# Kernel tuning notes

Hardware: AMD Instinct MI355X
Metric: run time of the kernel (lower is better)

The kernel has to match this reference:

```python
import jax, jax.numpy as jnp
import numpy as np

NUM_HEADS = 16


def setup_inputs() -> dict:
    key = jax.random.key(0)
    k1, k2, k3 = jax.random.split(key, 3)
    B, L, H = 2, 2048, 1024
    return {
        "key": jax.random.normal(k1, (B, L, H), dtype=jnp.float32),
        "W_ctx": jax.random.normal(k2, (H, H), dtype=jnp.float32) * (1.0 / np.sqrt(H)),
        "b_ctx": jax.random.normal(k3, (H,), dtype=jnp.float32) * 0.01,
    }


def reference(key, W_ctx, b_ctx):
    # Note: the torch module defines q/k/v Linear layers but never calls them
    # in forward(); it reshapes the raw input into heads directly.
    B, L, H = key.shape
    dh = H // NUM_HEADS
    # [B, L, H] -> [B, nh, L, dh]
    x = key.reshape(B, L, NUM_HEADS, dh).transpose(0, 2, 1, 3)
    # QK^T then scale by sqrt(head_dim) (key.shape[-1] after head split)
    scores = jnp.einsum("bhqd,bhkd->bhqk", x, x) * (1.0 / np.float32(np.sqrt(dh)))
    attn = jax.nn.softmax(scores, axis=-1)  # dropout p treated as eval/identity
    ctx = jnp.einsum("bhqk,bhkd->bhqd", attn, x)
    # [B, nh, L, dh] -> [B, L, H]
    ctx = ctx.transpose(0, 2, 1, 3).reshape(B, L, H)
    # context_transform: nn.Linear(H, H, bias=True)
    return ctx @ W_ctx.T + b_ctx
```

## Files before the change

### kernel.cpp

```cpp
#include <hip/hip_runtime.h>
#include <stdint.h>

#define NH     16
#define LSEQ   2048
#define DH     64
#define HDIM   1024
#define BATCH  2

typedef __attribute__((ext_vector_type(8))) short bf16x8;
typedef __attribute__((ext_vector_type(4))) short bf16x4;
typedef __attribute__((ext_vector_type(8))) unsigned short u16x8;
typedef __attribute__((ext_vector_type(4))) float f32x4;
typedef __attribute__((ext_vector_type(16))) float f32x16;

static __device__ inline unsigned short f2bs(float f) {
    union { float f; uint32_t u; } v; v.f = f;
    uint32_t u = v.u;
    return (unsigned short)((u + 0x7FFFu + ((u >> 16) & 1u)) >> 16);
}

static __device__ inline unsigned int cvtpk(float lo, float hi) {
    unsigned int r;
    asm("v_cvt_pk_bf16_f32 %0, %1, %2" : "=v"(r) : "v"(lo), "v"(hi));
    return r;
}
static __device__ inline void pl32swap(unsigned int &a, unsigned int &b) {
    asm volatile("v_permlane32_swap_b32 %0, %1" : "+v"(a), "+v"(b));
}

#define GLOAD_LDS(gp, lp) \
    __builtin_amdgcn_global_load_lds((const __attribute__((address_space(1))) void*)(gp), \
                                     (__attribute__((address_space(3))) void*)(lp), 16, 0, 0)

#define MFMA32(A, B, C) __builtin_amdgcn_mfma_f32_32x32x16_bf16((A), (B), (C), 0, 0, 0)

#define QK_SCALE 0.42466083f

__global__ __launch_bounds__(256) void prep_kernel(const float* __restrict__ x,
                                                   const float* __restrict__ W,
                                                   unsigned short* __restrict__ xb,
                                                   unsigned short* __restrict__ xt,
                                                   unsigned short* __restrict__ wbt) {
    const int lt = blockIdx.x, bh = blockIdx.y;
    const int bid = bh * 32 + lt;
    const int t = threadIdx.x;

    if (t < 128) {
        const int gid = bid * 128 + t;
        const int n  = gid >> 7;
        const int kc = gid & 127;
        const float* src = W + (size_t)n * 1024 + kc * 8;
        float4 f0 = *(const float4*)(src);
        float4 f1 = *(const float4*)(src + 4);
        u16x8 v;
        v[0]=f2bs(f0.x); v[1]=f2bs(f0.y); v[2]=f2bs(f0.z); v[3]=f2bs(f0.w);
        v[4]=f2bs(f1.x); v[5]=f2bs(f1.y); v[6]=f2bs(f1.z); v[7]=f2bs(f1.w);
        const int nt = n >> 7, rn = n & 127;
        const int kt = kc >> 3, c = kc & 7;
        *(u16x8*)(wbt + (((size_t)nt * 16 + kt) * 128 + rn) * 64 + ((c ^ (rn & 7)) * 8)) = v;
    }

    const int b = bh >> 4, h = bh & 15;
    const int r = t >> 2, cp = t & 3;

    __shared__ __align__(16) unsigned short Sm[64][72];

    const float* src = x + ((size_t)(b * LSEQ + lt * 64 + r)) * HDIM + h * DH + cp * 16;
    float4 f0 = *(const float4*)(src);
    float4 f1 = *(const float4*)(src + 4);
    float4 f2 = *(const float4*)(src + 8);
    float4 f3 = *(const float4*)(src + 12);
    u16x8 lo, hi;
    lo[0]=f2bs(f0.x); lo[1]=f2bs(f0.y); lo[2]=f2bs(f0.z); lo[3]=f2bs(f0.w);
    lo[4]=f2bs(f1.x); lo[5]=f2bs(f1.y); lo[6]=f2bs(f1.z); lo[7]=f2bs(f1.w);
    hi[0]=f2bs(f2.x); hi[1]=f2bs(f2.y); hi[2]=f2bs(f2.z); hi[3]=f2bs(f2.w);
    hi[4]=f2bs(f3.x); hi[5]=f2bs(f3.y); hi[6]=f2bs(f3.z); hi[7]=f2bs(f3.w);
    u16x8 slo, shi;
    slo[0]=f2bs(f0.x*QK_SCALE); slo[1]=f2bs(f0.y*QK_SCALE); slo[2]=f2bs(f0.z*QK_SCALE); slo[3]=f2bs(f0.w*QK_SCALE);
    slo[4]=f2bs(f1.x*QK_SCALE); slo[5]=f2bs(f1.y*QK_SCALE); slo[6]=f2bs(f1.z*QK_SCALE); slo[7]=f2bs(f1.w*QK_SCALE);
    shi[0]=f2bs(f2.x*QK_SCALE); shi[1]=f2bs(f2.y*QK_SCALE); shi[2]=f2bs(f2.z*QK_SCALE); shi[3]=f2bs(f2.w*QK_SCALE);
    shi[4]=f2bs(f3.x*QK_SCALE); shi[5]=f2bs(f3.y*QK_SCALE); shi[6]=f2bs(f3.z*QK_SCALE); shi[7]=f2bs(f3.w*QK_SCALE);

    {
        unsigned short* xrow = xb + (size_t)bid * 4096 + r * 64;
        const int xrs = (r & 7) * 8;
        *(u16x8*)(xrow + ((cp * 16 + 0) ^ xrs)) = slo;
        *(u16x8*)(xrow + ((cp * 16 + 8) ^ xrs)) = shi;
    }
    *(u16x8*)&Sm[r][cp * 16]     = lo;
    *(u16x8*)&Sm[r][cp * 16 + 8] = hi;
    __syncthreads();

    {
        const int d = t >> 2, part = (t & 3) * 16;
        unsigned short* vrow = xt + (size_t)bid * 4096 + d * 64;
        const int xrs = (d & 7) * 8;
        u16x8 g0, g1;
        #pragma unroll
        for (int i = 0; i < 8; ++i) g0[i] = Sm[part + i][d];
        #pragma unroll
        for (int i = 0; i < 8; ++i) g1[i] = Sm[part + 8 + i][d];
        *(u16x8*)(vrow + ((part + 0) ^ xrs)) = g0;
        *(u16x8*)(vrow + ((part + 8) ^ xrs)) = g1;
    }
}

__global__ __launch_bounds__(256) void attn_kernel(const unsigned short* __restrict__ xb,
                                                   const unsigned short* __restrict__ xt,
                                                   unsigned short* __restrict__ ctxt) {
    const int bh = blockIdx.x;
    const int qt = blockIdx.y;
    const int tid = threadIdx.x;
    const int w = tid >> 6, lane = tid & 63;
    const int l31 = lane & 31, hh = lane >> 5;

    __shared__ __align__(16) unsigned short KL[4][4096];
    __shared__ __align__(16) unsigned short VL[4][4096];

    const char* xbB = (const char*)(xb + (size_t)bh * 32 * 4096);
    const char* xtB = (const char*)(xt + (size_t)bh * 32 * 4096);

    bf16x8 qf[4];
    {
        const int qtile = qt * 2 + (w >> 1);
        const int rq = (w & 1) * 32 + l31;
        const char* qbase = xbB + (size_t)qtile * 8192 + rq * 128;
        const int qxr = (rq & 7) << 4;
        #pragma unroll
        for (int ds = 0; ds < 4; ++ds)
            qf[ds] = *(const bf16x8*)(qbase + ((ds * 32 + hh * 16) ^ qxr));
    }

    f32x16 accA, accB;
    #pragma unroll
    for (int r = 0; r < 16; ++r) { accA[r] = 0.f; accB[r] = 0.f; }
    float lp = 0.f;

    const int soff = tid * 16;
    #pragma unroll
    for (int j = 0; j < 2; ++j) {
        const char* kps = xbB + j * 8192;
        const char* vps = xtB + j * 8192;
        GLOAD_LDS(kps + soff,        (char*)KL[j] + soff);
        GLOAD_LDS(kps + 4096 + soff, (char*)KL[j] + 4096 + soff);
        GLOAD_LDS(vps + soff,        (char*)VL[j] + soff);
        GLOAD_LDS(vps + 4096 + soff, (char*)VL[j] + 4096 + soff);
    }
    asm volatile("s_waitcnt vmcnt(4)" ::: "memory");
    __builtin_amdgcn_s_barrier();

    const int kxr = (l31 & 7) << 4;

    for (int tt = 0; tt < 32; ++tt) {
        if (tt < 30) {
            const char* kps = xbB + (tt + 2) * 8192;
            const char* vps = xtB + (tt + 2) * 8192;
            char* kdst = (char*)KL[(tt + 2) & 3];
            char* vdst = (char*)VL[(tt + 2) & 3];
            GLOAD_LDS(kps + soff,        kdst + soff);
            GLOAD_LDS(kps + 4096 + soff, kdst + 4096 + soff);
            GLOAD_LDS(vps + soff,        vdst + soff);
            GLOAD_LDS(vps + 4096 + soff, vdst + 4096 + soff);
        }

        const char* kb0 = (const char*)KL[tt & 3] + l31 * 128;
        const char* kb1 = kb0 + 4096;
        f32x16 s0, s1;
        #pragma unroll
        for (int r = 0; r < 16; ++r) { s0[r] = 0.f; s1[r] = 0.f; }
        __builtin_amdgcn_s_setprio(1);
        #pragma unroll
        for (int ds = 0; ds < 4; ++ds) {
            const int off = (ds * 32 + hh * 16) ^ kxr;
            bf16x8 kfa = *(const bf16x8*)(kb0 + off);
            bf16x8 kfb = *(const bf16x8*)(kb1 + off);
            s0 = MFMA32(kfa, qf[ds], s0);
            s1 = MFMA32(kfb, qf[ds], s1);
        }
        __builtin_amdgcn_s_setprio(0);

        f32x16 e0, e1;
        {
            float ls = 0.f;
            #pragma unroll
            for (int r = 0; r < 16; ++r) {
                e0[r] = __builtin_amdgcn_exp2f(s0[r]);
                e1[r] = __builtin_amdgcn_exp2f(s1[r]);
                ls += e0[r] + e1[r];
            }
            lp += ls;
        }
        bf16x8 pa[4];
        #pragma unroll
        for (int ks = 0; ks < 4; ++ks) {
            const int r0 = (ks & 1) * 8;
            unsigned int x0, y0, x1, y1;
            if (ks < 2) {
                x0 = cvtpk(e0[r0 + 0], e0[r0 + 1]);
                y0 = cvtpk(e0[r0 + 4], e0[r0 + 5]);
                x1 = cvtpk(e0[r0 + 2], e0[r0 + 3]);
                y1 = cvtpk(e0[r0 + 6], e0[r0 + 7]);
            } else {
                x0 = cvtpk(e1[r0 + 0], e1[r0 + 1]);
                y0 = cvtpk(e1[r0 + 4], e1[r0 + 5]);
                x1 = cvtpk(e1[r0 + 2], e1[r0 + 3]);
                y1 = cvtpk(e1[r0 + 6], e1[r0 + 7]);
            }
            pl32swap(x0, y0);
            pl32swap(x1, y1);
            union { unsigned int u[4]; bf16x8 v; } pu;
            pu.u[0] = x0; pu.u[1] = x1; pu.u[2] = y0; pu.u[3] = y1;
            pa[ks] = pu.v;
        }

        if (tt < 30) {
            asm volatile("s_waitcnt vmcnt(4)" ::: "memory");
        } else {
            asm volatile("s_waitcnt vmcnt(0)" ::: "memory");
        }
        __builtin_amdgcn_s_barrier();

        const char* vb0 = (const char*)VL[tt & 3] + l31 * 128;
        const char* vb1 = vb0 + 4096;
        __builtin_amdgcn_s_setprio(1);
        #pragma unroll
        for (int ks = 0; ks < 4; ++ks) {
            const int off = (ks * 32 + hh * 16) ^ kxr;
            bf16x8 vfa = *(const bf16x8*)(vb0 + off);
            bf16x8 vfb = *(const bf16x8*)(vb1 + off);
            accA = MFMA32(pa[ks], vfa, accA);
            accB = MFMA32(pa[ks], vfb, accB);
        }
        __builtin_amdgcn_s_setprio(0);
    }

    lp += __shfl_xor(lp, 32);
    const float inv = 1.0f / lp;
    __syncthreads();
    float* invL = (float*)KL;
    invL[w * 32 + l31] = inv;
    __syncthreads();

    const int b = bh >> 4, hd = bh & 15;
    const int mt = b * 16 + qt;
    unsigned short* tbase = ctxt + ((size_t)mt * 16 + hd) * 128 * 64;
    const int col0 = l31, col1 = 32 + l31;
    const int c80 = col0 >> 3, c81 = col1 >> 3, ce = col0 & 7;
    #pragma unroll
    for (int r = 0; r < 16; ++r) {
        const int crow = (r & 3) + 8 * (r >> 2) + 4 * hh;
        const float iv = invL[w * 32 + crow];
        const int rr = w * 32 + crow;
        unsigned short* rowp = tbase + rr * 64;
        const int sw = rr & 7;
        rowp[((c80 ^ sw) * 8) + ce] = f2bs(accA[r] * iv);
        rowp[((c81 ^ sw) * 8) + ce] = f2bs(accB[r] * iv);
    }
}

__global__ __launch_bounds__(256) void proj_kernel(const unsigned short* __restrict__ ctxt,
                                                   const unsigned short* __restrict__ wbt,
                                                   const float* __restrict__ bias,
                                                   float* __restrict__ out) {
    const int ntb = blockIdx.x;
    const int mtb = blockIdx.y;
    const int tid = threadIdx.x;
    const int w = tid >> 6, lane = tid & 63;
    const int la = lane & 15, quad = lane >> 4;
    const int wm = (w >> 1) * 64, wn = (w & 1) * 64;

    __shared__ __align__(16) unsigned short As[2][8192];
    __shared__ __align__(16) unsigned short Bs[2][8192];

    const unsigned short* abase = ctxt + (size_t)mtb * 16 * 8192;
    const unsigned short* bbase = wbt  + (size_t)ntb * 16 * 8192;

    const int sw0 = ((quad)     ^ (la & 7)) * 8;
    const int sw1 = ((quad + 4) ^ (la & 7)) * 8;

    const f32x4 fzero = {0.f, 0.f, 0.f, 0.f};
    f32x4 acc[4][4];
    #pragma unroll
    for (int i = 0; i < 4; ++i)
        #pragma unroll
        for (int j = 0; j < 4; ++j) acc[i][j] = fzero;

    #pragma unroll
    for (int j = 0; j < 4; ++j) {
        const int fc = j * 256 + tid;
        GLOAD_LDS((const char*)abase + fc * 16, (char*)As[0] + fc * 16);
        GLOAD_LDS((const char*)bbase + fc * 16, (char*)Bs[0] + fc * 16);
    }
    __syncthreads();

    for (int kt = 0; kt < 16; ++kt) {
        if (kt < 15) {
            const char* asrc = (const char*)(abase + (kt + 1) * 8192);
            const char* bsrc = (const char*)(bbase + (kt + 1) * 8192);
            char* adst = (char*)As[(kt + 1) & 1];
            char* bdst = (char*)Bs[(kt + 1) & 1];
            #pragma unroll
            for (int j = 0; j < 4; ++j) {
                const int fc = j * 256 + tid;
                GLOAD_LDS(asrc + fc * 16, adst + fc * 16);
                GLOAD_LDS(bsrc + fc * 16, bdst + fc * 16);
            }
        }

        const unsigned short* Ab = As[kt & 1];
        const unsigned short* Bb = Bs[kt & 1];
        #pragma unroll
        for (int ks2 = 0; ks2 < 2; ++ks2) {
            const int sw = ks2 ? sw1 : sw0;
            bf16x8 af[4], bfr[4];
            #pragma unroll
            for (int mt = 0; mt < 4; ++mt) af[mt]  = *(const bf16x8*)&Ab[(wm + mt * 16 + la) * 64 + sw];
            #pragma unroll
            for (int nt = 0; nt < 4; ++nt) bfr[nt] = *(const bf16x8*)&Bb[(wn + nt * 16 + la) * 64 + sw];
            #pragma unroll
            for (int mt = 0; mt < 4; ++mt)
                #pragma unroll
                for (int nt = 0; nt < 4; ++nt)
                    acc[mt][nt] = __builtin_amdgcn_mfma_f32_16x16x32_bf16(af[mt], bfr[nt], acc[mt][nt], 0, 0, 0);
        }
        __syncthreads();
    }

    const int m0 = mtb * 128, n0 = ntb * 128;
    #pragma unroll
    for (int nt = 0; nt < 4; ++nt) {
        const int n = n0 + wn + nt * 16 + la;
        const float bv = bias[n];
        #pragma unroll
        for (int mt = 0; mt < 4; ++mt)
            #pragma unroll
            for (int r = 0; r < 4; ++r) {
                const int m = m0 + wm + mt * 16 + quad * 4 + r;
                out[(size_t)m * HDIM + n] = acc[mt][nt][r] + bv;
            }
    }
}

extern "C" void kernel_launch(void* const* d_in, const int* in_sizes, int n_in,
                              void* d_out, int out_size, void* d_ws, size_t ws_size,
                              hipStream_t stream) {
    const float* x    = (const float*)d_in[0];
    const float* W    = (const float*)d_in[1];
    const float* bias = (const float*)d_in[2];
    float* out = (float*)d_out;

    unsigned short* ctxt = (unsigned short*)d_ws;
    unsigned short* xbp  = (unsigned short*)((char*)d_ws + ( 8u << 20));
    unsigned short* xtp  = (unsigned short*)((char*)d_ws + (16u << 20));
    unsigned short* wbt  = (unsigned short*)((char*)d_ws + (24u << 20));

    prep_kernel<<<dim3(32, 32), 256, 0, stream>>>(x, W, xbp, xtp, wbt);
    attn_kernel<<<dim3(32, 16), 256, 0, stream>>>(xbp, xtp, ctxt);
    proj_kernel<<<dim3(8, 32), 256, 0, stream>>>(ctxt, wbt, bias, out);
}
```

Measured before the change: 144.3 us.

## Load K/V fragments directly from global in MFMA-ready layout, drop LDS staging

The prep kernel now writes K and V^T in a fragment-major layout so each lane can load its MFMA operands straight from global memory with contiguous 16-byte reads. The attention kernel drops the LDS ring buffer, the async global-to-LDS copies and the per-tile barriers. The softmax row sum is now computed with an extra MFMA against a ones vector instead of scalar adds and a shuffle. Occupancy is hinted at 3 blocks per SM. This relies on L2/cache for K/V reuse across the four waves and loses explicit prefetch overlap, and it adds one MFMA per step for the row sum.

Result: no change. 142.8 us (-1.0%).

```diff
diff --git a/kernel.cpp b/kernel.cpp
--- a/kernel.cpp
+++ b/kernel.cpp
@@ -8,7 +8,6 @@
 #define BATCH  2
 
 typedef __attribute__((ext_vector_type(8))) short bf16x8;
-typedef __attribute__((ext_vector_type(4))) short bf16x4;
 typedef __attribute__((ext_vector_type(8))) unsigned short u16x8;
 typedef __attribute__((ext_vector_type(4))) float f32x4;
 typedef __attribute__((ext_vector_type(16))) float f32x16;
@@ -82,10 +81,10 @@
     shi[4]=f2bs(f3.x*QK_SCALE); shi[5]=f2bs(f3.y*QK_SCALE); shi[6]=f2bs(f3.z*QK_SCALE); shi[7]=f2bs(f3.w*QK_SCALE);
 
     {
-        unsigned short* xrow = xb + (size_t)bid * 4096 + r * 64;
-        const int xrs = (r & 7) * 8;
-        *(u16x8*)(xrow + ((cp * 16 + 0) ^ xrs)) = slo;
-        *(u16x8*)(xrow + ((cp * 16 + 8) ^ xrs)) = shi;
+        unsigned short* xbase = xb + (size_t)bh * 131072
+                              + ((size_t)lt * 2 + (r >> 5)) * 2048 + cp * 512 + (r & 31) * 8;
+        *(u16x8*)(xbase)       = slo;
+        *(u16x8*)(xbase + 256) = shi;
     }
     *(u16x8*)&Sm[r][cp * 16]     = lo;
     *(u16x8*)&Sm[r][cp * 16 + 8] = hi;
@@ -93,118 +92,98 @@
 
     {
         const int d = t >> 2, part = (t & 3) * 16;
-        unsigned short* vrow = xt + (size_t)bid * 4096 + d * 64;
-        const int xrs = (d & 7) * 8;
+        unsigned short* vbase = xt + (size_t)bh * 131072 + (size_t)lt * 4096
+                              + (d >> 5) * 2048 + (part >> 4) * 512 + (d & 31) * 8;
         u16x8 g0, g1;
         #pragma unroll
         for (int i = 0; i < 8; ++i) g0[i] = Sm[part + i][d];
         #pragma unroll
         for (int i = 0; i < 8; ++i) g1[i] = Sm[part + 8 + i][d];
-        *(u16x8*)(vrow + ((part + 0) ^ xrs)) = g0;
-        *(u16x8*)(vrow + ((part + 8) ^ xrs)) = g1;
-    }
-}
-
-__global__ __launch_bounds__(256) void attn_kernel(const unsigned short* __restrict__ xb,
-                                                   const unsigned short* __restrict__ xt,
-                                                   unsigned short* __restrict__ ctxt) {
+        *(u16x8*)(vbase)       = g0;
+        *(u16x8*)(vbase + 256) = g1;
+    }
+}
+
+__global__ __launch_bounds__(256, 3) void attn_kernel(const unsigned short* __restrict__ xb,
+                                                      const unsigned short* __restrict__ xt,
+                                                      unsigned short* __restrict__ ctxt) {
     const int bh = blockIdx.x;
     const int qt = blockIdx.y;
     const int tid = threadIdx.x;
     const int w = tid >> 6, lane = tid & 63;
     const int l31 = lane & 31, hh = lane >> 5;
 
-    __shared__ __align__(16) unsigned short KL[4][4096];
-    __shared__ __align__(16) unsigned short VL[4][4096];
-
-    const char* xbB = (const char*)(xb + (size_t)bh * 32 * 4096);
-    const char* xtB = (const char*)(xt + (size_t)bh * 32 * 4096);
+    const char* xbB = (const char*)(xb + (size_t)bh * 131072);
+    const char* xtB = (const char*)(xt + (size_t)bh * 131072);
 
     bf16x8 qf[4];
     {
-        const int qtile = qt * 2 + (w >> 1);
-        const int rq = (w & 1) * 32 + l31;
-        const char* qbase = xbB + (size_t)qtile * 8192 + rq * 128;
-        const int qxr = (rq & 7) << 4;
+        const char* qbase = xbB + (size_t)(qt * 4 + w) * 4096 + lane * 16;
         #pragma unroll
         for (int ds = 0; ds < 4; ++ds)
-            qf[ds] = *(const bf16x8*)(qbase + ((ds * 32 + hh * 16) ^ qxr));
-    }
-
-    f32x16 accA, accB;
-    #pragma unroll
-    for (int r = 0; r < 16; ++r) { accA[r] = 0.f; accB[r] = 0.f; }
-    float lp = 0.f;
-
-    const int soff = tid * 16;
-    #pragma unroll
-    for (int j = 0; j < 2; ++j) {
-        const char* kps = xbB + j * 8192;
-        const char* vps = xtB + j * 8192;
-        GLOAD_LDS(kps + soff,        (char*)KL[j] + soff);
-        GLOAD_LDS(kps + 4096 + soff, (char*)KL[j] + 4096 + soff);
-        GLOAD_LDS(vps + soff,        (char*)VL[j] + soff);
-        GLOAD_LDS(vps + 4096 + soff, (char*)VL[j] + 4096 + soff);
-    }
-    asm volatile("s_waitcnt vmcnt(4)" ::: "memory");
-    __builtin_amdgcn_s_barrier();
-
-    const int kxr = (l31 & 7) << 4;
+            qf[ds] = *(const bf16x8*)(qbase + ds * 1024);
+    }
+
+    bf16x8 ones;
+    #pragma unroll
+    for (int i = 0; i < 8; ++i) ones[i] = (short)0x3F80;
+
+    f32x16 accA, accB, accS;
+    #pragma unroll
+    for (int r = 0; r < 16; ++r) { accA[r] = 0.f; accB[r] = 0.f; accS[r] = 0.f; }
+
+    const char* ka = xbB + lane * 16;
+    const char* va = xtB + lane * 16;
 
     for (int tt = 0; tt < 32; ++tt) {
-        if (tt < 30) {
-            const char* kps = xbB + (tt + 2) * 8192;
-            const char* vps = xtB + (tt + 2) * 8192;
-            char* kdst = (char*)KL[(tt + 2) & 3];
-            char* vdst = (char*)VL[(tt + 2) & 3];
-            GLOAD_LDS(kps + soff,        kdst + soff);
-            GLOAD_LDS(kps + 4096 + soff, kdst + 4096 + soff);
-            GLOAD_LDS(vps + soff,        vdst + soff);
-            GLOAD_LDS(vps + 4096 + soff, vdst + 4096 + soff);
-        }
-
-        const char* kb0 = (const char*)KL[tt & 3] + l31 * 128;
-        const char* kb1 = kb0 + 4096;
+        bf16x8 kfa[4], kfb[4];
+        #pragma unroll
+        for (int ds = 0; ds < 4; ++ds) {
+            kfa[ds] = *(const bf16x8*)(ka + ds * 1024);
+            kfb[ds] = *(const bf16x8*)(ka + 4096 + ds * 1024);
+        }
+
         f32x16 s0, s1;
         #pragma unroll
         for (int r = 0; r < 16; ++r) { s0[r] = 0.f; s1[r] = 0.f; }
         __builtin_amdgcn_s_setprio(1);
         #pragma unroll
         for (int ds = 0; ds < 4; ++ds) {
-            const int off = (ds * 32 + hh * 16) ^ kxr;
-            bf16x8 kfa = *(const bf16x8*)(kb0 + off);
-            bf16x8 kfb = *(const bf16x8*)(kb1 + off);
-            s0 = MFMA32(kfa, qf[ds], s0);
-            s1 = MFMA32(kfb, qf[ds], s1);
+            s0 = MFMA32(kfa[ds], qf[ds], s0);
+            s1 = MFMA32(kfb[ds], qf[ds], s1);
         }
         __builtin_amdgcn_s_setprio(0);
 
-        f32x16 e0, e1;
-        {
-            float ls = 0.f;
-            #pragma unroll
-            for (int r = 0; r < 16; ++r) {
-                e0[r] = __builtin_amdgcn_exp2f(s0[r]);
-                e1[r] = __builtin_amdgcn_exp2f(s1[r]);
-                ls += e0[r] + e1[r];
-            }
-            lp += ls;
-        }
+        bf16x8 vfa[4], vfb[4];
+        #pragma unroll
+        for (int ks = 0; ks < 4; ++ks) {
+            vfa[ks] = *(const bf16x8*)(va + ks * 1024);
+            vfb[ks] = *(const bf16x8*)(va + 4096 + ks * 1024);
+        }
+        ka += 8192;
+        va += 8192;
+
+        #pragma unroll
+        for (int r = 0; r < 16; ++r) {
+            s0[r] = __builtin_amdgcn_exp2f(s0[r]);
+            s1[r] = __builtin_amdgcn_exp2f(s1[r]);
+        }
+
         bf16x8 pa[4];
         #pragma unroll
         for (int ks = 0; ks < 4; ++ks) {
             const int r0 = (ks & 1) * 8;
             unsigned int x0, y0, x1, y1;
             if (ks < 2) {
-                x0 = cvtpk(e0[r0 + 0], e0[r0 + 1]);
-                y0 = cvtpk(e0[r0 + 4], e0[r0 + 5]);
-                x1 = cvtpk(e0[r0 + 2], e0[r0 + 3]);
-                y1 = cvtpk(e0[r0 + 6], e0[r0 + 7]);
+                x0 = cvtpk(s0[r0 + 0], s0[r0 + 1]);
+                y0 = cvtpk(s0[r0 + 4], s0[r0 + 5]);
+                x1 = cvtpk(s0[r0 + 2], s0[r0 + 3]);
+                y1 = cvtpk(s0[r0 + 6], s0[r0 + 7]);
             } else {
-                x0 = cvtpk(e1[r0 + 0], e1[r0 + 1]);
-                y0 = cvtpk(e1[r0 + 4], e1[r0 + 5]);
-                x1 = cvtpk(e1[r0 + 2], e1[r0 + 3]);
-                y1 = cvtpk(e1[r0 + 6], e1[r0 + 7]);
+                x0 = cvtpk(s1[r0 + 0], s1[r0 + 1]);
+                y0 = cvtpk(s1[r0 + 4], s1[r0 + 5]);
+                x1 = cvtpk(s1[r0 + 2], s1[r0 + 3]);
+                y1 = cvtpk(s1[r0 + 6], s1[r0 + 7]);
             }
             pl32swap(x0, y0);
             pl32swap(x1, y1);
@@ -213,43 +192,24 @@
             pa[ks] = pu.v;
         }
 
-        if (tt < 30) {
-            asm volatile("s_waitcnt vmcnt(4)" ::: "memory");
-        } else {
-            asm volatile("s_waitcnt vmcnt(0)" ::: "memory");
-        }
-        __builtin_amdgcn_s_barrier();
-
-        const char* vb0 = (const char*)VL[tt & 3] + l31 * 128;
-        const char* vb1 = vb0 + 4096;
         __builtin_amdgcn_s_setprio(1);
         #pragma unroll
         for (int ks = 0; ks < 4; ++ks) {
-            const int off = (ks * 32 + hh * 16) ^ kxr;
-            bf16x8 vfa = *(const bf16x8*)(vb0 + off);
-            bf16x8 vfb = *(const bf16x8*)(vb1 + off);
-            accA = MFMA32(pa[ks], vfa, accA);
-            accB = MFMA32(pa[ks], vfb, accB);
+            accA = MFMA32(pa[ks], vfa[ks], accA);
+            accB = MFMA32(pa[ks], vfb[ks], accB);
+            accS = MFMA32(pa[ks], ones, accS);
         }
         __builtin_amdgcn_s_setprio(0);
     }
-
-    lp += __shfl_xor(lp, 32);
-    const float inv = 1.0f / lp;
-    __syncthreads();
-    float* invL = (float*)KL;
-    invL[w * 32 + l31] = inv;
-    __syncthreads();
 
     const int b = bh >> 4, hd = bh & 15;
     const int mt = b * 16 + qt;
     unsigned short* tbase = ctxt + ((size_t)mt * 16 + hd) * 128 * 64;
-    const int col0 = l31, col1 = 32 + l31;
-    const int c80 = col0 >> 3, c81 = col1 >> 3, ce = col0 & 7;
+    const int c80 = l31 >> 3, c81 = 4 + (l31 >> 3), ce = l31 & 7;
     #pragma unroll
     for (int r = 0; r < 16; ++r) {
+        const float iv = 1.0f / accS[r];
         const int crow = (r & 3) + 8 * (r >> 2) + 4 * hh;
-        const float iv = invL[w * 32 + crow];
         const int rr = w * 32 + crow;
         unsigned short* rowp = tbase + rr * 64;
         const int sw = rr & 7;
```
